# Kernel tuning notes

Measured on AMD Instinct MI355X. Metric: run time of the kernel, lower is better.

## Reference

```python
import jax, jax.numpy as jnp
import numpy as np

N_NODES, SEQ_LEN, IN_CH, HID, OUT_CH, N_EDGES = 10000, 12, 16, 64, 1, 160000


def setup_inputs() -> dict:
    key = jax.random.key(0)
    ks = jax.random.split(key, 16)
    s = 1.0 / np.sqrt(HID)
    u = lambda k, shape: jax.random.uniform(k, shape, jnp.float32, -s, s)
    return {
        "x_seq": jax.random.normal(ks[0], (1, SEQ_LEN, N_NODES, IN_CH), jnp.float32),
        "edge_index": jax.random.randint(ks[1], (2, N_EDGES), 0, N_NODES, jnp.int32),
        "gcn_w": jax.random.normal(ks[2], (IN_CH, HID), jnp.float32) / np.sqrt(IN_CH),
        "gcn_b": jnp.zeros((HID,), jnp.float32),
        "w_ih0": u(ks[3], (3 * HID, HID)),
        "w_hh0": u(ks[4], (3 * HID, HID)),
        "b_ih0": u(ks[5], (3 * HID,)),
        "b_hh0": u(ks[6], (3 * HID,)),
        "w_ih1": u(ks[7], (3 * HID, HID)),
        "w_hh1": u(ks[8], (3 * HID, HID)),
        "b_ih1": u(ks[9], (3 * HID,)),
        "b_hh1": u(ks[10], (3 * HID,)),
        "attn_w": u(ks[11], (HID, 1)),
        "attn_b": u(ks[12], (1,)),
        "fc_w": u(ks[13], (HID, OUT_CH)),
        "fc_b": u(ks[14], (OUT_CH,)),
    }


def _gcn_all_t(x_ntf, edge_index, w, b):
    # x_ntf: (N, T, F). Symmetric-normalized GCNConv with self loops (PyG default),
    # applied to every timestep at once (edge structure is static).
    n = x_ntf.shape[0]
    loop = jnp.arange(n, dtype=edge_index.dtype)
    src = jnp.concatenate([edge_index[0], loop])
    dst = jnp.concatenate([edge_index[1], loop])
    deg = jax.ops.segment_sum(jnp.ones_like(src, dtype=x_ntf.dtype), dst, num_segments=n)
    dis = jax.lax.rsqrt(deg)  # deg >= 1 thanks to self loops
    norm = dis[src] * dis[dst]  # (E+N,)
    msg = x_ntf[src] * norm[:, None, None]  # (E+N, T, F)
    agg = jax.ops.segment_sum(msg, dst, num_segments=n)  # (N, T, F)
    return agg @ w + b  # (N, T, H)


def _gru_layer(x, w_ih, w_hh, b_ih, b_hh):
    # x: (B, T, Hin) batch_first; PyTorch GRU cell equations, h0 = 0.
    bsz, _, _ = x.shape
    h_dim = w_hh.shape[1]
    xi = x @ w_ih.T + b_ih  # (B, T, 3H), precomputed input projections

    def step(h, xt):
        gh = h @ w_hh.T + b_hh
        ir, iz, in_ = jnp.split(xt, 3, axis=-1)
        hr, hz, hn = jnp.split(gh, 3, axis=-1)
        r = jax.nn.sigmoid(ir + hr)
        z = jax.nn.sigmoid(iz + hz)
        n = jnp.tanh(in_ + r * hn)
        h_new = (1.0 - z) * n + z * h
        return h_new, h_new

    h0 = jnp.zeros((bsz, h_dim), x.dtype)
    _, hs = jax.lax.scan(step, h0, jnp.swapaxes(xi, 0, 1))  # (T, B, H)
    return jnp.swapaxes(hs, 0, 1)


def reference(x_seq, edge_index, gcn_w, gcn_b, w_ih0, w_hh0, b_ih0, b_hh0,
              w_ih1, w_hh1, b_ih1, b_hh1, attn_w, attn_b, fc_w, fc_b):
    batch, seq_len, num_nodes, _ = x_seq.shape  # batch == 1 (see notes)
    # (B, T, N, F) -> (N, T, F)
    x_ntf = jnp.swapaxes(x_seq[0], 0, 1)
    gcn_out = jax.nn.relu(_gcn_all_t(x_ntf, edge_index, gcn_w, gcn_b))  # (N, T, H)
    # gru_input: (B*N, T, H); dropout between GRU layers disabled (inference)
    h1 = _gru_layer(gcn_out, w_ih0, w_hh0, b_ih0, b_hh0)
    gru_out = _gru_layer(h1, w_ih1, w_hh1, b_ih1, b_hh1)  # (N, T, H)
    attn_scores = jax.nn.softmax(gru_out @ attn_w + attn_b, axis=1)  # (N, T, 1)
    context = jnp.sum(attn_scores * gru_out, axis=1)  # (N, H)
    residual = (context @ fc_w + fc_b).reshape(batch, num_nodes, -1)
    last_known = x_seq[:, -1, :, 0][..., None]  # (B, N, 1)
    return last_known + residual
```

## Files before the change

### kernel.cpp

```cpp
#include <hip/hip_runtime.h>
#include <hip/hip_bf16.h>
#include <hip/hip_fp16.h>

#define N_NODES 10000
#define SEQ_T 12
#define IN_CH 16
#define HID 64
#define N_EDGES 160000
#define CAP 96
#define PB 0xAAAAAAAAu

typedef __attribute__((ext_vector_type(8))) short short8;
typedef __attribute__((ext_vector_type(4))) float floatx4;

__device__ __forceinline__ float frcp(float x){ return __builtin_amdgcn_rcpf(x); }
__device__ __forceinline__ float sigmf(float x){ return frcp(1.0f + __expf(-x)); }
__device__ __forceinline__ float tanh_fast(float x){ return 1.0f - 2.0f * frcp(1.0f + __expf(2.0f * x)); }
__device__ __forceinline__ unsigned short f2bf(float f){
  union { float f; unsigned int u; } c; c.f = f;
  unsigned int u = c.u;
  return (unsigned short)((u + 0x7FFFu + ((u >> 16) & 1u)) >> 16);
}
__device__ __forceinline__ unsigned short f2h(float f){
  _Float16 h = (_Float16)f; unsigned short u; __builtin_memcpy(&u, &h, 2); return u;
}
__device__ __forceinline__ __half2 u32h2(unsigned int u){
  __half2 h; __builtin_memcpy(&h, &u, 4); return h;
}
__device__ __forceinline__ unsigned int cvt_pk_bf16(float a, float b){
  unsigned int r;
  asm("v_cvt_pk_bf16_f32 %0, %1, %2" : "=v"(r) : "v"(a), "v"(b));
  return r;
}


__global__ void k_fill(const int* __restrict__ ei, unsigned int* __restrict__ cnt,
                       int* __restrict__ csr,
                       const float* __restrict__ wih0, const float* __restrict__ whh0,
                       const float* __restrict__ wih1, const float* __restrict__ whh1,
                       unsigned short* __restrict__ wF,
                       const float* __restrict__ x, unsigned short* __restrict__ xT){
  int i = blockIdx.x * 256 + threadIdx.x;
  if (i < 49152){
    int p = i / 12288, ii = i - p * 12288;
    const float* sp = (p & 2) ? ((p & 1) ? whh1 : wih1) : ((p & 1) ? whh0 : wih0);
    int e = ii & 7, l = (ii >> 3) & 63, jk = ii >> 9;
    int kt = jk / 12, jt = jk - kt * 12;
    int j = (l & 15) + 16 * jt;
    int k = ((l >> 4) * 8) + e + 32 * kt;
    wF[i] = f2bf(sp[j * 64 + k]);
  }
  {
    int n = i >> 4, ch = i & 15;
    const float* xp = x + (size_t)n * IN_CH + ch;
    unsigned short tmp[SEQ_T];
    #pragma unroll
    for (int t = 0; t < SEQ_T; ++t) tmp[t] = f2h(xp[(size_t)t * N_NODES * IN_CH]);
    unsigned short* dp = xT + (size_t)n * 192 + ch * 12;
    *(ushort4*)(dp)     = make_ushort4(tmp[0], tmp[1], tmp[2],  tmp[3]);
    *(ushort4*)(dp + 4) = make_ushort4(tmp[4], tmp[5], tmp[6],  tmp[7]);
    *(ushort4*)(dp + 8) = make_ushort4(tmp[8], tmp[9], tmp[10], tmp[11]);
  }
  int s = ei[i], d = ei[N_EDGES + i];
  unsigned int pos = atomicAdd(&cnt[d], 1u) - PB;
  if (pos < CAP) csr[d * CAP + pos] = s;
}

__global__ __launch_bounds__(256, 3) void k_fused(
    const float* __restrict__ x, const unsigned short* __restrict__ xT,
    const unsigned int* __restrict__ cnt, const int* __restrict__ csr,
    const float* __restrict__ gcn_w, const float* __restrict__ gcn_b,
    const unsigned short* __restrict__ wF,
    const float* __restrict__ bih0, const float* __restrict__ bhh0,
    const float* __restrict__ bih1, const float* __restrict__ bhh1,
    const float* __restrict__ attn_w, const float* __restrict__ fc_w,
    const float* __restrict__ fc_b, float* __restrict__ out){
  __shared__ union {
    struct {
      int2  eLDS[16][16];
      unsigned short smB[SEQ_T][32][8];
    } A;
    struct {
      unsigned short HL[2][16][72];
      unsigned short h1[2][16][72];
      float scdc[SEQ_T][2][16];
    } B;
  } U;
  __shared__ unsigned short gout[SEQ_T][1024];
  __shared__ float biasL[2][4][64];

  const int tid = threadIdx.x;
  const int blk = blockIdx.x;
  const int w = tid >> 6;
  const int l = tid & 63;
  const int c = l & 15;
  const int q = l >> 4;
  const int hbase = 16 * w + 4 * q;

  if (tid < 128){
    int ly = tid >> 6, hh = tid & 63;
    const float* bi = ly ? bih1 : bih0;
    const float* bh = ly ? bhh1 : bhh0;
    biasL[ly][0][hh] = bi[hh] + bh[hh];
    biasL[ly][1][hh] = bi[64 + hh] + bh[64 + hh];
    biasL[ly][2][hh] = bi[128 + hh];
    biasL[ly][3][hh] = bh[128 + hh];
  }

  short8 aW = (short8){0, 0, 0, 0, 0, 0, 0, 0};
  if (l < 32){
    int jj = (l & 15) + 16 * w;
    #pragma unroll
    for (int e = 0; e < 8; ++e){
      int k = (l >> 4) * 8 + e;
      aW[e] = (short)f2bf(gcn_w[k * HID + jj]);
    }
  }
  floatx4 gb = *(const floatx4*)(gcn_b + hbase);

  {
    const int g = tid >> 4, ch = tid & 15;
    const int dst = blk * 16 + g;
    const int degF = (int)(cnt[dst] - PB);
    int deg = degF > CAP ? CAP : degF;
    float selfdis = rsqrtf((float)degF + 1.0f);
    __half2 ah0, ah1, ah2, ah3, ah4, ah5;
    {
      const uint2* xs = (const uint2*)(const void*)(xT + (size_t)dst * 192 + ch * 12);
      uint2 a = xs[0], b = xs[1], cc = xs[2];
      __half2 sd2 = __float2half2_rn(selfdis);
      ah0 = __hmul2(sd2, u32h2(a.x));  ah1 = __hmul2(sd2, u32h2(a.y));
      ah2 = __hmul2(sd2, u32h2(b.x));  ah3 = __hmul2(sd2, u32h2(b.y));
      ah4 = __hmul2(sd2, u32h2(cc.x)); ah5 = __hmul2(sd2, u32h2(cc.y));
    }
    for (int base = 0; base < deg; base += 16){
      int ep = base + ch;
      int2 ev = make_int2(0, 0);
      if (ep < deg){
        int s = csr[dst * CAP + ep];
        ev = make_int2(s, __float_as_int(rsqrtf((float)(cnt[s] - PB) + 1.0f)));
      }
      U.A.eLDS[g][ch] = ev;
      int c2 = deg - base; if (c2 > 16) c2 = 16;
      #pragma unroll 8
      for (int j = 0; j < c2; ++j){
        int2 e2 = U.A.eLDS[g][j];
        __half2 wh = __float2half2_rn(__int_as_float(e2.y));
        const uint2* xp = (const uint2*)(const void*)(xT + (size_t)e2.x * 192 + ch * 12);
        uint2 a = xp[0], b = xp[1], cc = xp[2];
        ah0 = __hfma2(wh, u32h2(a.x),  ah0); ah1 = __hfma2(wh, u32h2(a.y),  ah1);
        ah2 = __hfma2(wh, u32h2(b.x),  ah2); ah3 = __hfma2(wh, u32h2(b.y),  ah3);
        ah4 = __hfma2(wh, u32h2(cc.x), ah4); ah5 = __hfma2(wh, u32h2(cc.y), ah5);
      }
    }
    const int lp = (ch >> 3) * 16 + g, ep2 = ch & 7;
    float fv[SEQ_T];
    fv[0]  = __low2float(ah0); fv[1]  = __high2float(ah0);
    fv[2]  = __low2float(ah1); fv[3]  = __high2float(ah1);
    fv[4]  = __low2float(ah2); fv[5]  = __high2float(ah2);
    fv[6]  = __low2float(ah3); fv[7]  = __high2float(ah3);
    fv[8]  = __low2float(ah4); fv[9]  = __high2float(ah4);
    fv[10] = __low2float(ah5); fv[11] = __high2float(ah5);
    #pragma unroll
    for (int t = 0; t < SEQ_T; ++t)
      U.A.smB[t][lp][ep2] = f2bf(selfdis * fv[t]);
    __syncthreads();
  }

  {
    const int sec = (2 * w + (q >> 1)) & 3;
    const int goff = (w >> 1) * 512 + (c + 16 * sec) * 8 + (q & 1) * 4;
    #pragma unroll
    for (int t = 0; t < SEQ_T; ++t){
      short8 xb = (short8){0, 0, 0, 0, 0, 0, 0, 0};
      if (l < 32) xb = *(const short8*)&U.A.smB[t][l][0];
      floatx4 aC = gb;
      aC = __builtin_amdgcn_mfma_f32_16x16x32_bf16(aW, xb, aC, 0, 0, 0);
      unsigned int plo = cvt_pk_bf16(fmaxf(aC[0], 0.0f), fmaxf(aC[1], 0.0f));
      unsigned int phi = cvt_pk_bf16(fmaxf(aC[2], 0.0f), fmaxf(aC[3], 0.0f));
      *(uint2*)(void*)(&gout[t][goff]) = make_uint2(plo, phi);
    }
    __syncthreads();
  }

  short8 bw0[2][3][2], bw1[2][3][2];
  #pragma unroll
  for (int g2 = 0; g2 < 2; ++g2)
    #pragma unroll
    for (int s = 0; s < 3; ++s)
      #pragma unroll
      for (int kt = 0; kt < 2; ++kt){
        int jt = w + 4 * s;
        bw0[g2][s][kt] = *(const short8*)(wF + ((((size_t)g2 * 2 + kt) * 12 + jt) * 64 + l) * 8);
        bw1[g2][s][kt] = *(const short8*)(wF + ((((size_t)(2 + g2) * 2 + kt) * 12 + jt) * 64 + l) * 8);
      }
  short8 bwA[2];
  #pragma unroll
  for (int kt = 0; kt < 2; ++kt){
    short8 v;
    #pragma unroll
    for (int e = 0; e < 8; ++e){
      int k = q * 8 + e + 32 * kt;
      float f = (c == 0) ? attn_w[k] : (c == 1) ? fc_w[k] : 0.0f;
      v[e] = (short)f2bf(f);
    }
    bwA[kt] = v;
  }

  float hp0[4] = {0.f, 0.f, 0.f, 0.f};
  float hp1[4] = {0.f, 0.f, 0.f, 0.f};
  #pragma unroll 1
  for (int i = 0; i <= SEQ_T; ++i){
    if (i < SEQ_T){
      short8 xa0 = *(const short8*)&gout[i][l * 8];
      short8 xa1 = *(const short8*)&gout[i][512 + l * 8];
      floatx4 aR  = *(const floatx4*)&biasL[0][0][hbase];
      floatx4 aZ  = *(const floatx4*)&biasL[0][1][hbase];
      floatx4 aNx = *(const floatx4*)&biasL[0][2][hbase];
      floatx4 aNh = *(const floatx4*)&biasL[0][3][hbase];
      if (i > 0){
        short8 ha0 = *(const short8*)&U.B.HL[(i - 1) & 1][c][8 * q];
        short8 ha1 = *(const short8*)&U.B.HL[(i - 1) & 1][c][8 * q + 32];
        aR  = __builtin_amdgcn_mfma_f32_16x16x32_bf16(bw0[1][0][0], ha0, aR, 0, 0, 0);
        aR  = __builtin_amdgcn_mfma_f32_16x16x32_bf16(bw0[1][0][1], ha1, aR, 0, 0, 0);
        aZ  = __builtin_amdgcn_mfma_f32_16x16x32_bf16(bw0[1][1][0], ha0, aZ, 0, 0, 0);
        aZ  = __builtin_amdgcn_mfma_f32_16x16x32_bf16(bw0[1][1][1], ha1, aZ, 0, 0, 0);
        aNh = __builtin_amdgcn_mfma_f32_16x16x32_bf16(bw0[1][2][0], ha0, aNh, 0, 0, 0);
        aNh = __builtin_amdgcn_mfma_f32_16x16x32_bf16(bw0[1][2][1], ha1, aNh, 0, 0, 0);
      }
      aR  = __builtin_amdgcn_mfma_f32_16x16x32_bf16(bw0[0][0][0], xa0, aR, 0, 0, 0);
      aR  = __builtin_amdgcn_mfma_f32_16x16x32_bf16(bw0[0][0][1], xa1, aR, 0, 0, 0);
      aZ  = __builtin_amdgcn_mfma_f32_16x16x32_bf16(bw0[0][1][0], xa0, aZ, 0, 0, 0);
      aZ  = __builtin_amdgcn_mfma_f32_16x16x32_bf16(bw0[0][1][1], xa1, aZ, 0, 0, 0);
      aNx = __builtin_amdgcn_mfma_f32_16x16x32_bf16(bw0[0][2][0], xa0, aNx, 0, 0, 0);
      aNx = __builtin_amdgcn_mfma_f32_16x16x32_bf16(bw0[0][2][1], xa1, aNx, 0, 0, 0);
      float h4[4];
      #pragma unroll
      for (int r = 0; r < 4; ++r){
        float rr = sigmf(aR[r]);
        float zz = sigmf(aZ[r]);
        float nn = tanh_fast(aNx[r] + rr * aNh[r]);
        h4[r] = nn + zz * (hp0[r] - nn);
        hp0[r] = h4[r];
      }
      *(uint2*)(void*)(&U.B.HL[i & 1][c][hbase]) =
          make_uint2(cvt_pk_bf16(h4[0], h4[1]), cvt_pk_bf16(h4[2], h4[3]));
    }
    if (i >= 1){
      int t = i - 1;
      int pr = t & 1;
      short8 xb0 = *(const short8*)&U.B.HL[pr][c][8 * q];
      short8 xb1 = *(const short8*)&U.B.HL[pr][c][8 * q + 32];
      floatx4 aR  = *(const floatx4*)&biasL[1][0][hbase];
      floatx4 aZ  = *(const floatx4*)&biasL[1][1][hbase];
      floatx4 aNx = *(const floatx4*)&biasL[1][2][hbase];
      floatx4 aNh = *(const floatx4*)&biasL[1][3][hbase];
      if (t > 0){
        short8 hb0 = *(const short8*)&U.B.h1[pr][c][8 * q];
        short8 hb1 = *(const short8*)&U.B.h1[pr][c][8 * q + 32];
        aR  = __builtin_amdgcn_mfma_f32_16x16x32_bf16(bw1[1][0][0], hb0, aR, 0, 0, 0);
        aR  = __builtin_amdgcn_mfma_f32_16x16x32_bf16(bw1[1][0][1], hb1, aR, 0, 0, 0);
        aZ  = __builtin_amdgcn_mfma_f32_16x16x32_bf16(bw1[1][1][0], hb0, aZ, 0, 0, 0);
        aZ  = __builtin_amdgcn_mfma_f32_16x16x32_bf16(bw1[1][1][1], hb1, aZ, 0, 0, 0);
        aNh = __builtin_amdgcn_mfma_f32_16x16x32_bf16(bw1[1][2][0], hb0, aNh, 0, 0, 0);
        aNh = __builtin_amdgcn_mfma_f32_16x16x32_bf16(bw1[1][2][1], hb1, aNh, 0, 0, 0);
        if (w == (t & 3)){
          floatx4 aA = (floatx4){0.f, 0.f, 0.f, 0.f};
          aA = __builtin_amdgcn_mfma_f32_16x16x32_bf16(bwA[0], hb0, aA, 0, 0, 0);
          aA = __builtin_amdgcn_mfma_f32_16x16x32_bf16(bwA[1], hb1, aA, 0, 0, 0);
          if (q == 0){
            U.B.scdc[t - 1][0][c] = aA[0];
            U.B.scdc[t - 1][1][c] = aA[1];
          }
        }
      }
      aR  = __builtin_amdgcn_mfma_f32_16x16x32_bf16(bw1[0][0][0], xb0, aR, 0, 0, 0);
      aR  = __builtin_amdgcn_mfma_f32_16x16x32_bf16(bw1[0][0][1], xb1, aR, 0, 0, 0);
      aZ  = __builtin_amdgcn_mfma_f32_16x16x32_bf16(bw1[0][1][0], xb0, aZ, 0, 0, 0);
      aZ  = __builtin_amdgcn_mfma_f32_16x16x32_bf16(bw1[0][1][1], xb1, aZ, 0, 0, 0);
      aNx = __builtin_amdgcn_mfma_f32_16x16x32_bf16(bw1[0][2][0], xb0, aNx, 0, 0, 0);
      aNx = __builtin_amdgcn_mfma_f32_16x16x32_bf16(bw1[0][2][1], xb1, aNx, 0, 0, 0);
      float h4[4];
      #pragma unroll
      for (int r = 0; r < 4; ++r){
        float rr = sigmf(aR[r]);
        float zz = sigmf(aZ[r]);
        float nn = tanh_fast(aNx[r] + rr * aNh[r]);
        h4[r] = nn + zz * (hp1[r] - nn);
        hp1[r] = h4[r];
      }
      *(uint2*)(void*)(&U.B.h1[1 - pr][c][hbase]) =
          make_uint2(cvt_pk_bf16(h4[0], h4[1]), cvt_pk_bf16(h4[2], h4[3]));
    }
    __syncthreads();
  }

  if (w == 0){
    short8 hL0 = *(const short8*)&U.B.h1[0][c][8 * q];
    short8 hL1 = *(const short8*)&U.B.h1[0][c][8 * q + 32];
    floatx4 aA = (floatx4){0.f, 0.f, 0.f, 0.f};
    aA = __builtin_amdgcn_mfma_f32_16x16x32_bf16(bwA[0], hL0, aA, 0, 0, 0);
    aA = __builtin_amdgcn_mfma_f32_16x16x32_bf16(bwA[1], hL1, aA, 0, 0, 0);
    if (q == 0){
      U.B.scdc[SEQ_T - 1][0][c] = aA[0];
      U.B.scdc[SEQ_T - 1][1][c] = aA[1];
    }
    int gn = blk * 16 + l;
    if (l < 16){
      float sc[SEQ_T], dc[SEQ_T];
      #pragma unroll
      for (int t = 0; t < SEQ_T; ++t){ sc[t] = U.B.scdc[t][0][l]; dc[t] = U.B.scdc[t][1][l]; }
      float m = sc[0];
      #pragma unroll
      for (int t = 1; t < SEQ_T; ++t) m = fmaxf(m, sc[t]);
      float den = 0.0f, num = 0.0f;
      #pragma unroll
      for (int t = 0; t < SEQ_T; ++t){
        float p = __expf(sc[t] - m);
        den += p;
        num = fmaf(p, dc[t], num);
      }
      float y = fc_b[0] + num * frcp(den);
      float last = x[((size_t)(SEQ_T - 1) * N_NODES + gn) * IN_CH];
      out[gn] = last + y;
    }
  }
}

extern "C" void kernel_launch(void* const* d_in, const int* in_sizes, int n_in,
                              void* d_out, int out_size, void* d_ws, size_t ws_size,
                              hipStream_t stream){
  const float* x = (const float*)d_in[0];
  const int* ei  = (const int*)d_in[1];
  char* ws = (char*)d_ws;
  unsigned int*   cnt = (unsigned int*)(ws);
  int*            csr = (int*)(ws + 40960);
  unsigned short* wF  = (unsigned short*)(ws + 3880960);
  unsigned short* xT  = (unsigned short*)(ws + 3979264);

  k_fill<<<625, 256, 0, stream>>>(ei, cnt, csr,
      (const float*)d_in[4], (const float*)d_in[5],
      (const float*)d_in[8], (const float*)d_in[9], wF,
      x, xT);
  k_fused<<<625, 256, 0, stream>>>(
      x, xT, cnt, csr,
      (const float*)d_in[2], (const float*)d_in[3], wF,
      (const float*)d_in[6],  (const float*)d_in[7],
      (const float*)d_in[10], (const float*)d_in[11],
      (const float*)d_in[12], (const float*)d_in[14], (const float*)d_in[15],
      (float*)d_out);
}
```

Before: 134.4 us.

## Merge fill and fused kernels into one launch with a global atomic barrier

Folds the CSR-build, weight-repack and x-transpose kernel into the start of the main kernel and separates the phases with a grid-wide spin barrier on an atomic counter. This is meant to remove the second kernel launch and the gap between the two kernels. It relies on all 625 blocks being co-resident (3 blocks per CU at 256 threads), or the spin loop deadlocks. It also moves the attention-score MFMA to wave 0 on every step instead of rotating it across waves.

```diff
diff --git a/kernel.cpp b/kernel.cpp
--- a/kernel.cpp
+++ b/kernel.cpp
@@ -33,44 +33,15 @@
   return r;
 }
 
-
-__global__ void k_fill(const int* __restrict__ ei, unsigned int* __restrict__ cnt,
-                       int* __restrict__ csr,
-                       const float* __restrict__ wih0, const float* __restrict__ whh0,
-                       const float* __restrict__ wih1, const float* __restrict__ whh1,
-                       unsigned short* __restrict__ wF,
-                       const float* __restrict__ x, unsigned short* __restrict__ xT){
-  int i = blockIdx.x * 256 + threadIdx.x;
-  if (i < 49152){
-    int p = i / 12288, ii = i - p * 12288;
-    const float* sp = (p & 2) ? ((p & 1) ? whh1 : wih1) : ((p & 1) ? whh0 : wih0);
-    int e = ii & 7, l = (ii >> 3) & 63, jk = ii >> 9;
-    int kt = jk / 12, jt = jk - kt * 12;
-    int j = (l & 15) + 16 * jt;
-    int k = ((l >> 4) * 8) + e + 32 * kt;
-    wF[i] = f2bf(sp[j * 64 + k]);
-  }
-  {
-    int n = i >> 4, ch = i & 15;
-    const float* xp = x + (size_t)n * IN_CH + ch;
-    unsigned short tmp[SEQ_T];
-    #pragma unroll
-    for (int t = 0; t < SEQ_T; ++t) tmp[t] = f2h(xp[(size_t)t * N_NODES * IN_CH]);
-    unsigned short* dp = xT + (size_t)n * 192 + ch * 12;
-    *(ushort4*)(dp)     = make_ushort4(tmp[0], tmp[1], tmp[2],  tmp[3]);
-    *(ushort4*)(dp + 4) = make_ushort4(tmp[4], tmp[5], tmp[6],  tmp[7]);
-    *(ushort4*)(dp + 8) = make_ushort4(tmp[8], tmp[9], tmp[10], tmp[11]);
-  }
-  int s = ei[i], d = ei[N_EDGES + i];
-  unsigned int pos = atomicAdd(&cnt[d], 1u) - PB;
-  if (pos < CAP) csr[d * CAP + pos] = s;
-}
-
-__global__ __launch_bounds__(256, 3) void k_fused(
-    const float* __restrict__ x, const unsigned short* __restrict__ xT,
-    const unsigned int* __restrict__ cnt, const int* __restrict__ csr,
+__global__ __launch_bounds__(256, 3) void k_all(
+    const int* __restrict__ ei,
+    unsigned int* __restrict__ cnt, int* __restrict__ csr,
+    unsigned short* __restrict__ wF, unsigned short* __restrict__ xT,
+    unsigned int* __restrict__ gate,
+    const float* __restrict__ x,
     const float* __restrict__ gcn_w, const float* __restrict__ gcn_b,
-    const unsigned short* __restrict__ wF,
+    const float* __restrict__ wih0, const float* __restrict__ whh0,
+    const float* __restrict__ wih1, const float* __restrict__ whh1,
     const float* __restrict__ bih0, const float* __restrict__ bhh0,
     const float* __restrict__ bih1, const float* __restrict__ bhh1,
     const float* __restrict__ attn_w, const float* __restrict__ fc_w,
@@ -97,6 +68,33 @@
   const int q = l >> 4;
   const int hbase = 16 * w + 4 * q;
 
+  {
+    int i = blk * 256 + tid;
+    if (i < 49152){
+      int p = i / 12288, ii = i - p * 12288;
+      const float* sp = (p & 2) ? ((p & 1) ? whh1 : wih1) : ((p & 1) ? whh0 : wih0);
+      int e = ii & 7, ll = (ii >> 3) & 63, jk = ii >> 9;
+      int kt = jk / 12, jt = jk - kt * 12;
+      int j = (ll & 15) + 16 * jt;
+      int k = ((ll >> 4) * 8) + e + 32 * kt;
+      wF[i] = f2bf(sp[j * 64 + k]);
+    }
+    {
+      int n = i >> 4, ch = i & 15;
+      const float* xp = x + (size_t)n * IN_CH + ch;
+      unsigned short tmp[SEQ_T];
+      #pragma unroll
+      for (int t = 0; t < SEQ_T; ++t) tmp[t] = f2h(xp[(size_t)t * N_NODES * IN_CH]);
+      unsigned short* dp = xT + (size_t)n * 192 + ch * 12;
+      *(ushort4*)(dp)     = make_ushort4(tmp[0], tmp[1], tmp[2],  tmp[3]);
+      *(ushort4*)(dp + 4) = make_ushort4(tmp[4], tmp[5], tmp[6],  tmp[7]);
+      *(ushort4*)(dp + 8) = make_ushort4(tmp[8], tmp[9], tmp[10], tmp[11]);
+    }
+    int s = ei[i], d = ei[N_EDGES + i];
+    unsigned int pos = atomicAdd(&cnt[d], 1u) - PB;
+    if (pos < CAP) csr[d * CAP + pos] = s;
+  }
+
   if (tid < 128){
     int ly = tid >> 6, hh = tid & 63;
     const float* bi = ly ? bih1 : bih0;
@@ -106,7 +104,6 @@
     biasL[ly][2][hh] = bi[128 + hh];
     biasL[ly][3][hh] = bh[128 + hh];
   }
-
   short8 aW = (short8){0, 0, 0, 0, 0, 0, 0, 0};
   if (l < 32){
     int jj = (l & 15) + 16 * w;
@@ -117,6 +114,15 @@
     }
   }
   floatx4 gb = *(const floatx4*)(gcn_b + hbase);
+
+  __threadfence();
+  __syncthreads();
+  if (tid == 0){
+    atomicAdd(gate, 1u);
+    while (atomicAdd(gate, 0u) - PB < 625u) { }
+  }
+  __syncthreads();
+  __threadfence();
 
   {
     const int g = tid >> 4, ch = tid & 15;
@@ -264,7 +270,7 @@
         aZ  = __builtin_amdgcn_mfma_f32_16x16x32_bf16(bw1[1][1][1], hb1, aZ, 0, 0, 0);
         aNh = __builtin_amdgcn_mfma_f32_16x16x32_bf16(bw1[1][2][0], hb0, aNh, 0, 0, 0);
         aNh = __builtin_amdgcn_mfma_f32_16x16x32_bf16(bw1[1][2][1], hb1, aNh, 0, 0, 0);
-        if (w == (t & 3)){
+        if (w == 0){
           floatx4 aA = (floatx4){0.f, 0.f, 0.f, 0.f};
           aA = __builtin_amdgcn_mfma_f32_16x16x32_bf16(bwA[0], hb0, aA, 0, 0, 0);
           aA = __builtin_amdgcn_mfma_f32_16x16x32_bf16(bwA[1], hb1, aA, 0, 0, 0);
@@ -333,18 +339,17 @@
   const float* x = (const float*)d_in[0];
   const int* ei  = (const int*)d_in[1];
   char* ws = (char*)d_ws;
-  unsigned int*   cnt = (unsigned int*)(ws);
-  int*            csr = (int*)(ws + 40960);
-  unsigned short* wF  = (unsigned short*)(ws + 3880960);
-  unsigned short* xT  = (unsigned short*)(ws + 3979264);
-
-  k_fill<<<625, 256, 0, stream>>>(ei, cnt, csr,
-      (const float*)d_in[4], (const float*)d_in[5],
-      (const float*)d_in[8], (const float*)d_in[9], wF,
-      x, xT);
-  k_fused<<<625, 256, 0, stream>>>(
-      x, xT, cnt, csr,
-      (const float*)d_in[2], (const float*)d_in[3], wF,
+  unsigned int*   cnt  = (unsigned int*)(ws);
+  int*            csr  = (int*)(ws + 40960);
+  unsigned short* wF   = (unsigned short*)(ws + 3880960);
+  unsigned short* xT   = (unsigned short*)(ws + 3979264);
+  unsigned int*   gate = (unsigned int*)(ws + 7819264);
+
+  k_all<<<625, 256, 0, stream>>>(
+      ei, cnt, csr, wF, xT, gate, x,
+      (const float*)d_in[2],  (const float*)d_in[3],
+      (const float*)d_in[4],  (const float*)d_in[5],
+      (const float*)d_in[8],  (const float*)d_in[9],
       (const float*)d_in[6],  (const float*)d_in[7],
       (const float*)d_in[10], (const float*)d_in[11],
       (const float*)d_in[12], (const float*)d_in[14], (const float*)d_in[15],
```

Measured after the change: 285.8 us. +112.6%, slower.
